# Kernel optimization log

Hardware: AMD Instinct MI355X
Metric: run time of the kernel (lower is better)

The kernel has to match this reference:

```python
import jax, jax.numpy as jnp
import numpy as np

N_NODES = 500000
N_EDGES = 1000000
H = 128


def setup_inputs() -> dict:
    key = jax.random.key(0)
    ks = jax.random.split(key, 8)
    s = 1.0 / np.sqrt(H)
    return {
        "z": jax.random.normal(ks[0], (N_NODES, H), dtype=jnp.float32),
        "w1": jax.random.normal(ks[1], (H, H), dtype=jnp.float32) * s,
        "b1": jax.random.normal(ks[2], (H,), dtype=jnp.float32) * s,
        "w2": jax.random.normal(ks[3], (H, H), dtype=jnp.float32) * s,
        "b2": jax.random.normal(ks[4], (H,), dtype=jnp.float32) * s,
        "wb": jax.random.normal(ks[5], (1, H, H), dtype=jnp.float32) * s,
        "bb": jax.random.normal(ks[6], (1,), dtype=jnp.float32) * s,
        "pot_arcs": jax.random.randint(ks[7], (N_EDGES, 2), 0, N_NODES, dtype=jnp.int64),
    }


def reference(z, w1, b1, w2, b2, wb, bb, pot_arcs):
    # Gather head/dep node embeddings per candidate arc: [E, H]
    x1 = z[pot_arcs[:, 0]]
    x2 = z[pot_arcs[:, 1]]
    # Per-node linear + relu (dropout is identity in eval mode)
    h1 = jax.nn.relu(x1 @ w1.T + b1)
    h2 = jax.nn.relu(x2 @ w2.T + b2)
    # Bilinear score: h1 @ W @ h2^T per edge, out_features=1
    score = jnp.einsum("eh,hk,ek->e", h1, wb[0], h2) + bb[0]
    return score
```

## Files before the change

### kernel.cpp

```cpp
#include <hip/hip_runtime.h>
#include <hip/hip_bf16.h>

#define HDIM 128

typedef short bf16x8 __attribute__((ext_vector_type(8)));
typedef short bf16x4 __attribute__((ext_vector_type(4)));
typedef unsigned short u16x8 __attribute__((ext_vector_type(8)));
typedef float f32x4 __attribute__((ext_vector_type(4)));

__device__ __forceinline__ short f2bf(float f) {
    __hip_bfloat16 h = __float2bfloat16(f);
    union { __hip_bfloat16 h; short s; } c; c.h = h; return c.s;
}
__device__ __forceinline__ float bf2f(unsigned short h) {
    union { unsigned u; float f; } c; c.u = ((unsigned)h) << 16; return c.f;
}
__device__ __forceinline__ bf16x8 pack8(float4 a, float4 b) {
    bf16x8 r;
    r[0] = f2bf(a.x); r[1] = f2bf(a.y); r[2] = f2bf(a.z); r[3] = f2bf(a.w);
    r[4] = f2bf(b.x); r[5] = f2bf(b.y); r[6] = f2bf(b.z); r[7] = f2bf(b.w);
    return r;
}

__device__ __forceinline__ void barrier_lds() {
    asm volatile("s_waitcnt lgkmcnt(0)" ::: "memory");
    __builtin_amdgcn_s_barrier();
    __builtin_amdgcn_sched_barrier(0);
}

__global__ __launch_bounds__(512, 4)
void node_phase(const float* __restrict__ z,
                const float* __restrict__ w1, const float* __restrict__ b1,
                const float* __restrict__ w2, const float* __restrict__ b2,
                const float* __restrict__ wb,
                unsigned short* __restrict__ g1, unsigned short* __restrict__ h2o,
                int N)
{
    __shared__ short zbb[2][4096];
    __shared__ short h1x[2][4096];
    __shared__ short h2x[2][4096];
    __shared__ short g1x[2][4096];

    const int t = threadIdx.x;
    const int lane = t & 63, wid = t >> 6;
    const int l15 = lane & 15, kgrp = lane >> 4;
    const int feat = wid * 16 + l15;

    bf16x8 w1f[4], w2f[4], wbf[4];
    {
        const float* w1r = w1 + (size_t)feat * HDIM;
        const float* w2r = w2 + (size_t)feat * HDIM;
#pragma unroll
        for (int kt = 0; kt < 4; ++kt) {
            int k0 = kt * 32 + kgrp * 8;
            w1f[kt] = pack8(*(const float4*)(w1r + k0), *(const float4*)(w1r + k0 + 4));
            w2f[kt] = pack8(*(const float4*)(w2r + k0), *(const float4*)(w2r + k0 + 4));
            bf16x8 r;
#pragma unroll
            for (int i = 0; i < 8; ++i) r[i] = f2bf(wb[(size_t)(k0 + i) * HDIM + feat]);
            wbf[kt] = r;
        }
    }
    f32x4 bias1, bias2;
#pragma unroll
    for (int r = 0; r < 4; ++r) {
        bias1[r] = b1[wid * 16 + kgrp * 4 + r];
        bias2[r] = b2[wid * 16 + kgrp * 4 + r];
    }

    const int srow = t >> 4;
    const int sp   = t & 15;
    const int sg   = sp ^ (srow & 7);

    const int ntiles = (N + 31) >> 5;
    const int myTiles = (ntiles > (int)blockIdx.x)
                      ? ((ntiles - 1 - (int)blockIdx.x) / (int)gridDim.x + 1) : 0;
    const int nit = myTiles + 2;
    const int ng = wid * 2 + (kgrp >> 1);

    if (myTiles > 0) {
        int row = (int)blockIdx.x * 32 + srow;
        int rc = row < N ? row : N - 1;
        const float* src = z + (size_t)rc * HDIM + sg * 8;
        *(bf16x8*)&zbb[0][t * 8] = pack8(*(const float4*)src, *(const float4*)(src + 4));
    }
    __syncthreads();

    for (int i = 0; i < nit; ++i) {
        const int cur = i & 1, prv = cur ^ 1;
        const int tvA = (int)blockIdx.x + i * (int)gridDim.x;
        const bool vA = (i < myTiles);
        const bool vB = (i >= 1) && (i - 1 < myTiles);
        const bool vG = (i >= 2) && (i - 2 < myTiles);
        const bool vP = (i + 1 < myTiles);

        float4 zn0, zn1;
        if (vP) {
            int row = (tvA + (int)gridDim.x) * 32 + srow;
            int rc = row < N ? row : N - 1;
            const float* src = z + (size_t)rc * HDIM + sg * 8;
            zn0 = *(const float4*)src;
            zn1 = *(const float4*)(src + 4);
        }
        if (vG) {
            int row = (tvA - 2 * (int)gridDim.x) * 32 + srow;
            u16x8 vv = *(const u16x8*)&g1x[prv][srow * 128 + sp * 8];
            if (row < N) *(u16x8*)&g1[(size_t)row * HDIM + (sp ^ (srow & 7)) * 8] = vv;
        }
        if (vB) {
            int row = (tvA - (int)gridDim.x) * 32 + srow;
            u16x8 vv = *(const u16x8*)&h2x[prv][srow * 128 + sp * 8];
            if (row < N) *(u16x8*)&h2o[(size_t)row * HDIM + (sp ^ (srow & 7)) * 8] = vv;
        }
        if (vA) {
#pragma unroll
            for (int gp = 0; gp < 2; ++gp) {
                const int m = gp * 16 + l15;
                bf16x8 zf[4];
#pragma unroll
                for (int kt = 0; kt < 4; ++kt) {
                    int pos = (kt * 4 + kgrp) ^ (m & 7);
                    zf[kt] = *(const bf16x8*)&zbb[cur][m * 128 + pos * 8];
                }
                f32x4 a1 = bias1, a3 = bias2;
#pragma unroll
                for (int kt = 0; kt < 4; ++kt) {
                    a1 = __builtin_amdgcn_mfma_f32_16x16x32_bf16(w1f[kt], zf[kt], a1, 0, 0, 0);
                    a3 = __builtin_amdgcn_mfma_f32_16x16x32_bf16(w2f[kt], zf[kt], a3, 0, 0, 0);
                }
                const int sidx = m * 128 + ((ng ^ (m & 7)) << 3) + ((kgrp & 1) << 2);
                bf16x4 h1v, h2v;
#pragma unroll
                for (int r = 0; r < 4; ++r) {
                    float x1 = a1[r] > 0.f ? a1[r] : 0.f;
                    float x2 = a3[r] > 0.f ? a3[r] : 0.f;
                    h1v[r] = f2bf(x1);
                    h2v[r] = f2bf(x2);
                }
                *(bf16x4*)&h1x[cur][sidx] = h1v;
                *(bf16x4*)&h2x[cur][sidx] = h2v;
            }
        }
        if (vB) {
#pragma unroll
            for (int gp = 0; gp < 2; ++gp) {
                const int m = gp * 16 + l15;
                f32x4 ag = (f32x4){0.f, 0.f, 0.f, 0.f};
#pragma unroll
                for (int kt = 0; kt < 4; ++kt) {
                    int pos = (kt * 4 + kgrp) ^ (m & 7);
                    bf16x8 bf = *(const bf16x8*)&h1x[prv][m * 128 + pos * 8];
                    ag = __builtin_amdgcn_mfma_f32_16x16x32_bf16(wbf[kt], bf, ag, 0, 0, 0);
                }
                const int sidx = m * 128 + ((ng ^ (m & 7)) << 3) + ((kgrp & 1) << 2);
                bf16x4 gv;
#pragma unroll
                for (int r = 0; r < 4; ++r) gv[r] = f2bf(ag[r]);
                *(bf16x4*)&g1x[cur][sidx] = gv;
            }
        }
        if (vP) {
            *(bf16x8*)&zbb[prv][t * 8] = pack8(zn0, zn1);
        }
        barrier_lds();
    }
}

__global__ void detect_idx64(const int* __restrict__ arcs, int* __restrict__ flag)
{
    int v = arcs[2 * threadIdx.x + 1];
    unsigned long long any = __ballot(v != 0);
    if (threadIdx.x == 0) *flag = (any == 0ull) ? 1 : 0;
}

__global__ __launch_bounds__(256, 8)
void edge_phase(const unsigned short* __restrict__ g1,
                const unsigned short* __restrict__ h2,
                const void* __restrict__ arcs,
                const int* __restrict__ flag,
                const float* __restrict__ bb,
                float* __restrict__ out, int E)
{
    const int t = threadIdx.x;
    const int sub = t & 15;
    const int e = blockIdx.x * 16 + (t >> 4);
    const int ec = e < E ? e : (E - 1);

    long long u, v;
    if (*flag) {
        const long long* a = (const long long*)arcs;
        u = a[2 * (size_t)ec]; v = a[2 * (size_t)ec + 1];
    } else {
        const int* a = (const int*)arcs;
        u = a[2 * (size_t)ec]; v = a[2 * (size_t)ec + 1];
    }

    u16x8 av = *(const u16x8*)(g1 + (size_t)u * HDIM + sub * 8);
    u16x8 bv = *(const u16x8*)(h2 + (size_t)v * HDIM + sub * 8);
    float s = 0.f;
#pragma unroll
    for (int i = 0; i < 8; ++i) s += bf2f(av[i]) * bf2f(bv[i]);

    s += __shfl_xor(s, 8, 16);
    s += __shfl_xor(s, 4, 16);
    s += __shfl_xor(s, 2, 16);
    s += __shfl_xor(s, 1, 16);

    if (sub == 0 && e < E) out[e] = s + bb[0];
}

extern "C" void kernel_launch(void* const* d_in, const int* in_sizes, int n_in,
                              void* d_out, int out_size, void* d_ws, size_t ws_size,
                              hipStream_t stream)
{
    const float* z  = (const float*)d_in[0];
    const float* w1 = (const float*)d_in[1];
    const float* b1 = (const float*)d_in[2];
    const float* w2 = (const float*)d_in[3];
    const float* b2 = (const float*)d_in[4];
    const float* wb = (const float*)d_in[5];
    const float* bb = (const float*)d_in[6];
    const void*  arcs = d_in[7];

    const int N = in_sizes[0] / HDIM;
    const int E = in_sizes[7] / 2;

    char* ws = (char*)d_ws;
    int* flag = (int*)ws;
    unsigned short* g1 = (unsigned short*)(ws + 256);
    unsigned short* h2 = g1 + (size_t)N * HDIM;

    detect_idx64<<<1, 64, 0, stream>>>((const int*)arcs, flag);

    node_phase<<<512, 512, 0, stream>>>(z, w1, b1, w2, b2, wb, g1, h2, N);

    int eblk = (E + 15) / 16;
    edge_phase<<<eblk, 256, 0, stream>>>(g1, h2, arcs, flag, bb, (float*)d_out, E);
}
```

Baseline: 186.7 us.

## Replace software-pipelined node phase with barrier-synchronized stages for higher occupancy

The node-phase kernel drops its three-stage software pipeline (prefetching z into registers, double-buffered z and h1 tiles) for a simpler per-tile flow: load z, barrier, compute h1/h2, barrier, compute g1. Output stores of the previous tile's h2 and g1 still overlap with the current tile. Shared memory per block shrinks, launch bounds go from 4 to 6 blocks per CU, and the grid grows from 512 to 768 blocks. The aim is to hide memory latency through occupancy rather than explicit prefetch, at the cost of an extra barrier per tile and an exposed global load before compute.

New measurement: 460.2 us. +146.5%, slower.

```diff
diff --git a/kernel.cpp b/kernel.cpp
--- a/kernel.cpp
+++ b/kernel.cpp
@@ -28,7 +28,7 @@
     __builtin_amdgcn_sched_barrier(0);
 }
 
-__global__ __launch_bounds__(512, 4)
+__global__ __launch_bounds__(512, 6)
 void node_phase(const float* __restrict__ z,
                 const float* __restrict__ w1, const float* __restrict__ b1,
                 const float* __restrict__ w2, const float* __restrict__ b2,
@@ -36,8 +36,8 @@
                 unsigned short* __restrict__ g1, unsigned short* __restrict__ h2o,
                 int N)
 {
-    __shared__ short zbb[2][4096];
-    __shared__ short h1x[2][4096];
+    __shared__ short zbb[4096];
+    __shared__ short h1x[4096];
     __shared__ short h2x[2][4096];
     __shared__ short g1x[2][4096];
 
@@ -75,42 +75,31 @@
     const int ntiles = (N + 31) >> 5;
     const int myTiles = (ntiles > (int)blockIdx.x)
                       ? ((ntiles - 1 - (int)blockIdx.x) / (int)gridDim.x + 1) : 0;
-    const int nit = myTiles + 2;
+    const int nit = myTiles + 1;
     const int ng = wid * 2 + (kgrp >> 1);
-
-    if (myTiles > 0) {
-        int row = (int)blockIdx.x * 32 + srow;
-        int rc = row < N ? row : N - 1;
-        const float* src = z + (size_t)rc * HDIM + sg * 8;
-        *(bf16x8*)&zbb[0][t * 8] = pack8(*(const float4*)src, *(const float4*)(src + 4));
-    }
-    __syncthreads();
 
     for (int i = 0; i < nit; ++i) {
         const int cur = i & 1, prv = cur ^ 1;
-        const int tvA = (int)blockIdx.x + i * (int)gridDim.x;
+        const int tA = (int)blockIdx.x + i * (int)gridDim.x;
         const bool vA = (i < myTiles);
-        const bool vB = (i >= 1) && (i - 1 < myTiles);
-        const bool vG = (i >= 2) && (i - 2 < myTiles);
-        const bool vP = (i + 1 < myTiles);
-
-        float4 zn0, zn1;
-        if (vP) {
-            int row = (tvA + (int)gridDim.x) * 32 + srow;
+        const bool vS = (i >= 1);
+
+        if (vA) {
+            int row = tA * 32 + srow;
             int rc = row < N ? row : N - 1;
             const float* src = z + (size_t)rc * HDIM + sg * 8;
-            zn0 = *(const float4*)src;
-            zn1 = *(const float4*)(src + 4);
-        }
-        if (vG) {
-            int row = (tvA - 2 * (int)gridDim.x) * 32 + srow;
-            u16x8 vv = *(const u16x8*)&g1x[prv][srow * 128 + sp * 8];
-            if (row < N) *(u16x8*)&g1[(size_t)row * HDIM + (sp ^ (srow & 7)) * 8] = vv;
-        }
-        if (vB) {
-            int row = (tvA - (int)gridDim.x) * 32 + srow;
-            u16x8 vv = *(const u16x8*)&h2x[prv][srow * 128 + sp * 8];
-            if (row < N) *(u16x8*)&h2o[(size_t)row * HDIM + (sp ^ (srow & 7)) * 8] = vv;
+            *(bf16x8*)&zbb[t * 8] = pack8(*(const float4*)src, *(const float4*)(src + 4));
+        }
+        barrier_lds();
+
+        if (vS) {
+            int row = (tA - (int)gridDim.x) * 32 + srow;
+            if (row < N) {
+                u16x8 hv = *(const u16x8*)&h2x[prv][srow * 128 + sp * 8];
+                u16x8 gv = *(const u16x8*)&g1x[prv][srow * 128 + sp * 8];
+                *(u16x8*)&h2o[(size_t)row * HDIM + (sp ^ (srow & 7)) * 8] = hv;
+                *(u16x8*)&g1[(size_t)row * HDIM + (sp ^ (srow & 7)) * 8] = gv;
+            }
         }
         if (vA) {
 #pragma unroll
@@ -120,7 +109,7 @@
 #pragma unroll
                 for (int kt = 0; kt < 4; ++kt) {
                     int pos = (kt * 4 + kgrp) ^ (m & 7);
-                    zf[kt] = *(const bf16x8*)&zbb[cur][m * 128 + pos * 8];
+                    zf[kt] = *(const bf16x8*)&zbb[m * 128 + pos * 8];
                 }
                 f32x4 a1 = bias1, a3 = bias2;
 #pragma unroll
@@ -137,11 +126,13 @@
                     h1v[r] = f2bf(x1);
                     h2v[r] = f2bf(x2);
                 }
-                *(bf16x4*)&h1x[cur][sidx] = h1v;
+                *(bf16x4*)&h1x[sidx] = h1v;
                 *(bf16x4*)&h2x[cur][sidx] = h2v;
             }
         }
-        if (vB) {
+        barrier_lds();
+
+        if (vA) {
 #pragma unroll
             for (int gp = 0; gp < 2; ++gp) {
                 const int m = gp * 16 + l15;
@@ -149,7 +140,7 @@
 #pragma unroll
                 for (int kt = 0; kt < 4; ++kt) {
                     int pos = (kt * 4 + kgrp) ^ (m & 7);
-                    bf16x8 bf = *(const bf16x8*)&h1x[prv][m * 128 + pos * 8];
+                    bf16x8 bf = *(const bf16x8*)&h1x[m * 128 + pos * 8];
                     ag = __builtin_amdgcn_mfma_f32_16x16x32_bf16(wbf[kt], bf, ag, 0, 0, 0);
                 }
                 const int sidx = m * 128 + ((ng ^ (m & 7)) << 3) + ((kgrp & 1) << 2);
@@ -159,10 +150,6 @@
                 *(bf16x4*)&g1x[cur][sidx] = gv;
             }
         }
-        if (vP) {
-            *(bf16x8*)&zbb[prv][t * 8] = pack8(zn0, zn1);
-        }
-        barrier_lds();
     }
 }
 
@@ -232,7 +219,7 @@
 
     detect_idx64<<<1, 64, 0, stream>>>((const int*)arcs, flag);
 
-    node_phase<<<512, 512, 0, stream>>>(z, w1, b1, w2, b2, wb, g1, h2, N);
+    node_phase<<<768, 512, 0, stream>>>(z, w1, b1, w2, b2, wb, g1, h2, N);
 
     int eblk = (E + 15) / 16;
     edge_phase<<<eblk, 256, 0, stream>>>(g1, h2, arcs, flag, bb, (float*)d_out, E);
```
